# Optimization experiments

Hardware: AMD Instinct MI355X
Metric: run time of the kernel (lower is better)

The kernel has to match this reference:

```python
import jax, jax.numpy as jnp
import numpy as np
from jax import lax

EPS = 1e-5
NBIT = 127.0  # 8-bit symmetric: 2^(8-1)-1

def ste_round(x):
    return x + lax.stop_gradient(jnp.round(x) - x)

def quant_act(x, rng_max):
    # symmetric fake-quant of activations with learned per-cluster range
    s = rng_max / NBIT
    xq = jnp.clip(ste_round(x / s), -NBIT, NBIT) * s
    return xq, s

def fold_bn(w, gamma, beta, mean, var):
    std = jnp.sqrt(var + EPS)
    scale = gamma / std
    w_f = w * scale[:, None, None, None]
    b_f = beta - mean * scale
    return w_f, b_f

def quant_weight(w):
    # per-output-channel symmetric quant
    s = jnp.max(jnp.abs(w), axis=(1, 2, 3), keepdims=True) / NBIT
    wq = jnp.clip(ste_round(w / s), -NBIT, NBIT) * s
    return wq, s.reshape(-1)

def conv(x, w, stride=1, groups=1, pad=0):
    return lax.conv_general_dilated(
        x, w, window_strides=(stride, stride),
        padding=((pad, pad), (pad, pad)),
        dimension_numbers=('NCHW', 'OIHW', 'NCHW'),
        feature_group_count=groups)

def setup_inputs() -> dict:
    key = jax.random.key(0)
    ks = jax.random.split(key, 24)
    B, Cin, H, W = 64, 96, 28, 28
    Cmid, Cout, NC = 576, 96, 4
    d = {}
    d['x'] = jax.random.normal(ks[0], (B, Cin, H, W), dtype=jnp.float32)
    # conv1: 1x1 expansion
    d['w1'] = jax.random.normal(ks[1], (Cmid, Cin, 1, 1), jnp.float32) * 0.1
    d['g1'] = jax.random.uniform(ks[2], (Cmid,), minval=0.5, maxval=1.5)
    d['b1'] = jax.random.normal(ks[3], (Cmid,)) * 0.1
    d['m1'] = jax.random.normal(ks[4], (Cmid,)) * 0.1
    d['v1'] = jax.random.uniform(ks[5], (Cmid,), minval=0.5, maxval=1.5)
    # conv2: 3x3 depthwise
    d['w2'] = jax.random.normal(ks[6], (Cmid, 1, 3, 3), jnp.float32) * 0.1
    d['g2'] = jax.random.uniform(ks[7], (Cmid,), minval=0.5, maxval=1.5)
    d['b2'] = jax.random.normal(ks[8], (Cmid,)) * 0.1
    d['m2'] = jax.random.normal(ks[9], (Cmid,)) * 0.1
    d['v2'] = jax.random.uniform(ks[10], (Cmid,), minval=0.5, maxval=1.5)
    # conv3: 1x1 projection
    d['w3'] = jax.random.normal(ks[11], (Cout, Cmid, 1, 1), jnp.float32) * 0.1
    d['g3'] = jax.random.uniform(ks[12], (Cout,), minval=0.5, maxval=1.5)
    d['b3'] = jax.random.normal(ks[13], (Cout,)) * 0.1
    d['m3'] = jax.random.normal(ks[14], (Cout,)) * 0.1
    d['v3'] = jax.random.uniform(ks[15], (Cout,), minval=0.5, maxval=1.5)
    # per-cluster learned activation ranges for the 4 QuantAct modules
    d['r0'] = jax.random.uniform(ks[16], (NC,), minval=2.0, maxval=8.0)
    d['r1'] = jax.random.uniform(ks[17], (NC,), minval=2.0, maxval=8.0)
    d['r2'] = jax.random.uniform(ks[18], (NC,), minval=2.0, maxval=8.0)
    d['r3'] = jax.random.uniform(ks[19], (NC,), minval=2.0, maxval=8.0)
    d['cluster'] = 2
    return d

def reference(x, w1, g1, b1, m1, v1, w2, g2, b2, m2, v2,
              w3, g3, b3, m3, v3, r0, r1, r2, r3, cluster):
    identity = x  # residual path (in==out, stride==1)
    # QuantAct -> conv1 (BN-folded, per-channel quant) -> ReLU6
    xq, s0 = quant_act(x, r0[cluster])
    w1f, bf1 = fold_bn(w1, g1, b1, m1, v1)
    w1q, ws1 = quant_weight(w1f)
    y = conv(xq, w1q) + bf1[None, :, None, None]
    y = jnp.clip(y, 0.0, 6.0)
    # QuantAct1 -> depthwise conv2 -> ReLU6
    yq, s1 = quant_act(y, r1[cluster])
    w2f, bf2 = fold_bn(w2, g2, b2, m2, v2)
    w2q, ws2 = quant_weight(w2f)
    y = conv(yq, w2q, stride=1, groups=w2.shape[0], pad=1) + bf2[None, :, None, None]
    y = jnp.clip(y, 0.0, 6.0)
    # QuantAct2 -> conv3 projection
    yq, s2 = quant_act(y, r2[cluster])
    w3f, bf3 = fold_bn(w3, g3, b3, m3, v3)
    w3q, ws3 = quant_weight(w3f)
    y = conv(yq, w3q) + bf3[None, :, None, None]
    # residual add, then int32 requant
    y = y + identity
    out, s3 = quant_act(y, r3[cluster])
    return out, s3
```

## Files before the change

kernel.cpp:

```cpp
#include <hip/hip_runtime.h>
#include <cstdint>
#include <cstddef>

typedef int   v4i __attribute__((ext_vector_type(4)));
typedef float v4f __attribute__((ext_vector_type(4)));
typedef unsigned int u32;

constexpr int B_   = 64;
constexpr int CIN  = 96;
constexpr int P_   = 784;
constexpr int CMID = 576;
constexpr int COUT = 96;
constexpr int NOUT = B_ * COUT * P_;
constexpr float NBITF = 127.0f;
constexpr float EPSF  = 1e-5f;
constexpr float MAGICF = 12582912.0f;
constexpr int   BIASI  = 0x4B400000;

constexpr int XKD = 36;
constexpr int XBD = 13 * XKD * 64;

__device__ __forceinline__ int dot3(u32 a, u32 w, int acc) {
#if __has_builtin(__builtin_amdgcn_sdot4)
    return __builtin_amdgcn_sdot4((int)a, (int)w, acc, false);
#else
    return acc + (int)(signed char)(a)        * (int)(signed char)(w)
               + (int)(signed char)(a >> 8)   * (int)(signed char)(w >> 8)
               + (int)(signed char)(a >> 16)  * (int)(signed char)(w >> 16);
#endif
}

__device__ __forceinline__ void tr4(u32 S0, u32 S1, u32 S2, u32 S3, u32 O[4]) {
    u32 u01 = __builtin_amdgcn_perm(S1, S0, 0x05010400u);
    u32 u23 = __builtin_amdgcn_perm(S3, S2, 0x05010400u);
    u32 v01 = __builtin_amdgcn_perm(S1, S0, 0x07030602u);
    u32 v23 = __builtin_amdgcn_perm(S3, S2, 0x07030602u);
    O[0] = __builtin_amdgcn_perm(u23, u01, 0x05040100u);
    O[1] = __builtin_amdgcn_perm(u23, u01, 0x07060302u);
    O[2] = __builtin_amdgcn_perm(v23, v01, 0x05040100u);
    O[3] = __builtin_amdgcn_perm(v23, v01, 0x07060302u);
}

__device__ __forceinline__ u32 pack4(u32 t0, u32 t1, u32 t2, u32 t3) {
    u32 p01 = __builtin_amdgcn_perm(t1, t0, 0x05010400u);
    u32 p23 = __builtin_amdgcn_perm(t3, t2, 0x05010400u);
    return __builtin_amdgcn_perm(p23, p01, 0x05040100u);
}

__global__ __launch_bounds__(256)
void prep_all(const float* __restrict__ x,
              const float* __restrict__ w1, const float* __restrict__ g1,
              const float* __restrict__ b1, const float* __restrict__ m1,
              const float* __restrict__ v1,
              const float* __restrict__ w2, const float* __restrict__ g2,
              const float* __restrict__ b2, const float* __restrict__ m2,
              const float* __restrict__ v2,
              const float* __restrict__ w3, const float* __restrict__ g3,
              const float* __restrict__ b3, const float* __restrict__ m3,
              const float* __restrict__ v3,
              const float* __restrict__ r0, const int* __restrict__ cluster,
              u32* __restrict__ x8t,
              int8_t* __restrict__ w1qp, float* __restrict__ ws1, float* __restrict__ bf1,
              v4i* __restrict__ w2pk, float* __restrict__ ws2, float* __restrict__ bf2,
              int8_t* __restrict__ w3qp, float* __restrict__ ws3, float* __restrict__ bf3)
{
    __shared__ u32 T[112 * 37];
    int tid = threadIdx.x;

    if (blockIdx.x < 448) {
        int pt0 = blockIdx.x % 7, b = blockIdx.x / 7;
        float inv_s0 = NBITF / r0[cluster[0]];

        for (int i = tid; i < 112 * 12; i += 256) {
            int row = i / 12, cpad = i - row * 12;
            T[row * 37 + 24 + cpad] = 0u;
        }
        for (int u = tid; u < 24 * 28; u += 256) {
            int pq = u % 28, icq = u / 28;
            int pxb = pt0 * 112 + pq * 4;
            int q[4][4];
            #pragma unroll
            for (int j = 0; j < 4; j++) {
                v4f xv = *(const v4f*)(x + ((size_t)b * CIN + icq * 4 + j) * P_ + pxb);
                #pragma unroll
                for (int i = 0; i < 4; i++)
                    q[j][i] = (int)fminf(fmaxf(rintf(xv[i] * inv_s0), -127.f), 127.f);
            }
            #pragma unroll
            for (int i = 0; i < 4; i++) {
                u32 t0 = __builtin_amdgcn_perm((u32)q[1][i], (u32)q[0][i], 0x00000400u);
                u32 t1 = __builtin_amdgcn_perm((u32)q[3][i], (u32)q[2][i], 0x00000400u);
                T[(pq * 4 + i) * 37 + icq] = __builtin_amdgcn_perm(t1, t0, 0x05040100u);
            }
        }
        __syncthreads();
        u32* gb = x8t + (size_t)b * XBD;
        for (int i = tid; i < XKD * 112; i += 256) {
            int icq = i / 112, pxo = i - icq * 112;
            int px = pt0 * 112 + pxo;
            gb[(((px >> 6) * XKD) + icq) * 64 + (px & 63)] = T[pxo * 37 + icq];
        }
        return;
    }

    int lane = tid & 63, wv = tid >> 6;
    int blk = (blockIdx.x - 448) * 4 + wv;

    const float *w, *g, *bb, *mm, *vv;
    int oc, K, which;
    if (blk < CMID)            { which = 0; w = w1; g = g1; bb = b1; mm = m1; vv = v1; oc = blk;            K = CIN;  }
    else if (blk < 2 * CMID)   { which = 1; w = w2; g = g2; bb = b2; mm = m2; vv = v2; oc = blk - CMID;     K = 9;    }
    else                       { which = 2; w = w3; g = g3; bb = b3; mm = m3; vv = v3; oc = blk - 2 * CMID; K = CMID; }

    float scale = g[oc] / sqrtf(vv[oc] + EPSF);

    float mx = 0.f;
    for (int k = lane; k < K; k += 64)
        mx = fmaxf(mx, fabsf(w[oc * K + k] * scale));
    #pragma unroll
    for (int off = 1; off < 64; off <<= 1)
        mx = fmaxf(mx, __shfl_xor(mx, off));

    float s = mx / NBITF;

    int myq = 0;
    for (int k = lane; k < K; k += 64) {
        float wf = w[oc * K + k] * scale;
        float q  = fminf(fmaxf(rintf(wf / s), -127.f), 127.f);
        if (which == 0)      w1qp[oc * 144 + k] = (int8_t)q;
        else if (which == 1) myq = (int)q;
        else                 w3qp[oc * 592 + k] = (int8_t)q;
    }
    if (which == 0 && lane < 12)
        ((u32*)(w1qp + oc * 144))[24 + lane] = 0u;
    if (which == 1) {
        u32 qq[9];
        #pragma unroll
        for (int t = 0; t < 9; t++) qq[t] = (u32)__shfl(myq, t, 64) & 0xffu;
        if (lane == 0) {
            v4i pk;
            pk[0] = (int)(qq[0] | (qq[1] << 8) | (qq[2] << 16));
            pk[1] = (int)(qq[3] | (qq[4] << 8) | (qq[5] << 16));
            pk[2] = (int)(qq[6] | (qq[7] << 8) | (qq[8] << 16));
            pk[3] = 0;
            w2pk[oc] = pk;
        }
    }
    if (lane == 0) {
        float bf = bb[oc] - mm[oc] * scale;
        if (which == 0)      { ws1[oc] = s; bf1[oc] = bf; }
        else if (which == 1) { ws2[oc] = s; bf2[oc] = bf; }
        else                 { ws3[oc] = s; bf3[oc] = bf; }
    }
}

__global__ __launch_bounds__(256)
void conv12v2(const u32* __restrict__ x8t, const int8_t* __restrict__ w1qp,
              const float* __restrict__ ws1, const float* __restrict__ bf1,
              const v4i* __restrict__ w2pk, const float* __restrict__ ws2,
              const float* __restrict__ bf2,
              const float* __restrict__ r0, const float* __restrict__ r1,
              const float* __restrict__ r2, const int* __restrict__ cluster,
              u32* __restrict__ y2px)
{
    __shared__ u32 y1w[192 * 34];

    int tid = threadIdx.x, b = blockIdx.y;
    int mt = blockIdx.x % 3, pt = blockIdx.x / 3;
    int p0 = pt * 64;
    int lane = tid & 63, wv = tid >> 6;
    int n = lane & 15, q4 = lane >> 4;
    int ocw = mt * 192 + wv * 48;

    int   c      = cluster[0];
    float s0     = r0[c] / NBITF;
    float s1     = r1[c] / NBITF;
    float inv_s1 = NBITF / r1[c];
    float inv_s2 = NBITF / r2[c];
    int   u1i    = (int)fminf(rintf(6.f * inv_s1), 127.f);
    int   u2i    = (int)fminf(rintf(6.f * inv_s2), 127.f);

    const u32* xb = x8t + (size_t)b * XBD;
    int abase[8];
    #pragma unroll
    for (int jm = 0; jm < 8; jm++) {
        int px = p0 - 32 + 16 * jm + n;
        px = min(max(px, 0), P_ - 1);
        abase[jm] = ((px >> 6) * XKD) * 64 + (px & 63);
    }

    v4i acc[3][8];
    #pragma unroll
    for (int jn = 0; jn < 3; jn++)
        #pragma unroll
        for (int jm = 0; jm < 8; jm++) acc[jn][jm] = (v4i){0, 0, 0, 0};

    const v4i* w4 = (const v4i*)w1qp;
    #pragma unroll
    for (int ks = 0; ks < 2; ks++) {
        v4i bfr[3];
        #pragma unroll
        for (int jn = 0; jn < 3; jn++) {
            int oc = ocw + 16 * jn + n;
            bfr[jn] = w4[oc * 9 + ks * 4 + q4];
        }
        int kb = (16 * ks + 4 * q4) * 64;
        #pragma unroll
        for (int jm = 0; jm < 8; jm++) {
            u32 d0 = xb[abase[jm] + kb];
            u32 d1 = xb[abase[jm] + kb + 64];
            u32 d2 = xb[abase[jm] + kb + 128];
            u32 d3 = xb[abase[jm] + kb + 192];
            v4i afr = (v4i){(int)d0, (int)d1, (int)d2, (int)d3};
            #pragma unroll
            for (int jn = 0; jn < 3; jn++)
                acc[jn][jm] = __builtin_amdgcn_mfma_i32_16x16x64_i8(afr, bfr[jn], acc[jn][jm], 0, 0, 0);
        }
    }

    #pragma unroll
    for (int jn = 0; jn < 3; jn++) {
        int   oc  = ocw + 16 * jn + n;
        int   chl = wv * 48 + 16 * jn + n;
        float scv = s0 * ws1[oc] * inv_s1;
        float bbv = bf1[oc] * inv_s1;
        #pragma unroll
        for (int jm = 0; jm < 8; jm++) {
            u32 t[4];
            #pragma unroll
            for (int r = 0; r < 4; r++) {
                int wpx = p0 - 32 + 16 * jm + 4 * q4 + r;
                float f = fmaf((float)acc[jn][jm][r], scv, bbv) + MAGICF;
                int v = min(max(__float_as_int(f), BIASI), BIASI + u1i);
                t[r] = ((unsigned)wpx < (unsigned)P_) ? (u32)v : (u32)BIASI;
            }
            y1w[chl * 34 + 4 * jm + q4] = pack4(t[0], t[1], t[2], t[3]);
        }
    }
    __syncthreads();

    int d0g = p0 >> 2;
    #pragma unroll
    for (int it = 0; it < 12; it++) {
        int u   = tid + 256 * it;
        int chl = u >> 4, dq = u & 15;
        int d   = d0g + dq;
        int gcol = d % 7;
        int base = chl * 34 + 8 + dq;

        u32 M[3][3];
        #pragma unroll
        for (int rr = 0; rr < 3; rr++) {
            int o = (rr - 1) * 7;
            M[rr][0] = (gcol == 0) ? 0u : y1w[base + o - 1];
            M[rr][1] = y1w[base + o];
            M[rr][2] = (gcol == 6) ? 0u : y1w[base + o + 1];
        }
        int ch = mt * 192 + chl;
        v4i wpk = w2pk[ch];
        int a0 = 0, a1 = 0, a2 = 0, a3 = 0;
        #pragma unroll
        for (int rr = 0; rr < 3; rr++) {
            u32 Dm1 = M[rr][0], D = M[rr][1], Dp1 = M[rr][2];
            u32 pk = (u32)((rr == 0) ? wpk[0] : (rr == 1) ? wpk[1] : wpk[2]);
            a0 = dot3(__builtin_amdgcn_alignbyte(D, Dm1, 3), pk, a0);
            a1 = dot3(D, pk, a1);
            a2 = dot3(__builtin_amdgcn_alignbyte(Dp1, D, 1), pk, a2);
            a3 = dot3(__builtin_amdgcn_alignbyte(Dp1, D, 2), pk, a3);
        }
        float scv = s1 * ws2[ch] * inv_s2;
        float bbv = bf2[ch] * inv_s2;
        int aa[4] = {a0, a1, a2, a3};
        u32 tq[4];
        #pragma unroll
        for (int i = 0; i < 4; i++) {
            float f = fmaf((float)aa[i], scv, bbv) + MAGICF;
            tq[i] = (u32)min(max(__float_as_int(f), BIASI), BIASI + u2i);
        }
        if (d < 196)
            y2px[(size_t)(b * CMID + ch) * 196 + d] = pack4(tq[0], tq[1], tq[2], tq[3]);
    }
}

__global__ __launch_bounds__(256)
void conv3s(const u32* __restrict__ y2px, const int8_t* __restrict__ w3qp,
            const float* __restrict__ ws3, const float* __restrict__ bf3,
            const float* __restrict__ x, const float* __restrict__ r2,
            const float* __restrict__ r3, const int* __restrict__ cluster,
            float* __restrict__ out)
{
    __shared__ u32 Bsh[144 * 67];

    int tid = threadIdx.x, b = blockIdx.y, pt = blockIdx.x;
    int p0d = pt * 16;

    int   c      = cluster[0];
    float s2     = r2[c] / NBITF;
    float s3     = r3[c] / NBITF;
    float inv_s3 = NBITF / r3[c];

    for (int u = tid; u < 2304; u += 256) {
        int pxq = u & 15, chq = u >> 4;
        u32 S[4];
        #pragma unroll
        for (int r = 0; r < 4; r++) {
            int col = min(p0d + pxq, 195);
            S[r] = y2px[(size_t)(b * CMID + 4 * chq + r) * 196 + col];
        }
        u32 O[4];
        tr4(S[0], S[1], S[2], S[3], O);
        #pragma unroll
        for (int k = 0; k < 4; k++)
            Bsh[chq * 67 + 4 * pxq + k] = O[k];
    }
    __syncthreads();

    int lane = tid & 63, wv = tid >> 6;
    int n = lane & 15, q4 = lane >> 4;
    int pxl = wv * 16 + n;

    v4i acc[6];
    #pragma unroll
    for (int i = 0; i < 6; i++) acc[i] = (v4i){0, 0, 0, 0};

    #pragma unroll
    for (int ks = 0; ks < 9; ks++) {
        int kr = 16 * ks + 4 * q4;
        u32 b0 = Bsh[(kr + 0) * 67 + pxl];
        u32 b1 = Bsh[(kr + 1) * 67 + pxl];
        u32 b2 = Bsh[(kr + 2) * 67 + pxl];
        u32 b3 = Bsh[(kr + 3) * 67 + pxl];
        v4i bfr = (v4i){(int)b0, (int)b1, (int)b2, (int)b3};
        #pragma unroll
        for (int i = 0; i < 6; i++) {
            v4i afr = *(const v4i*)(w3qp + (size_t)(i * 16 + n) * 592 + ks * 64 + q4 * 16);
            acc[i] = __builtin_amdgcn_mfma_i32_16x16x64_i8(afr, bfr, acc[i], 0, 0, 0);
        }
    }

    int px = pt * 64 + pxl;
    if (px < P_) {
        #pragma unroll
        for (int i = 0; i < 6; i++) {
            #pragma unroll
            for (int r = 0; r < 4; r++) {
                int oc = i * 16 + q4 * 4 + r;
                size_t gi = (size_t)(b * COUT + oc) * P_ + px;
                float v  = (float)acc[i][r] * (s2 * ws3[oc]) + bf3[oc] + x[gi];
                float f  = fmaf(v, inv_s3, MAGICF);
                int lvl  = min(max(__float_as_int(f) - BIASI, -127), 127);
                out[gi]  = (float)lvl * s3;
            }
        }
    }
    if (pt == 0 && b == 0 && tid == 0)
        out[NOUT] = s3;
}

extern "C" void kernel_launch(void* const* d_in, const int* in_sizes, int n_in,
                              void* d_out, int out_size, void* d_ws, size_t ws_size,
                              hipStream_t stream)
{
    const float* x  = (const float*)d_in[0];
    const float* w1 = (const float*)d_in[1];
    const float* g1 = (const float*)d_in[2];
    const float* b1 = (const float*)d_in[3];
    const float* m1 = (const float*)d_in[4];
    const float* v1 = (const float*)d_in[5];
    const float* w2 = (const float*)d_in[6];
    const float* g2 = (const float*)d_in[7];
    const float* b2 = (const float*)d_in[8];
    const float* m2 = (const float*)d_in[9];
    const float* v2 = (const float*)d_in[10];
    const float* w3 = (const float*)d_in[11];
    const float* g3 = (const float*)d_in[12];
    const float* b3 = (const float*)d_in[13];
    const float* m3 = (const float*)d_in[14];
    const float* v3 = (const float*)d_in[15];
    const float* r0 = (const float*)d_in[16];
    const float* r1 = (const float*)d_in[17];
    const float* r2 = (const float*)d_in[18];
    const float* r3 = (const float*)d_in[19];
    const int*   cl = (const int*)d_in[20];

    float* out = (float*)d_out;

    char*  ws  = (char*)d_ws;
    size_t off = 0;
    auto carve = [&](size_t bytes) {
        size_t cur = off;
        off = (off + bytes + 255) & ~(size_t)255;
        return (void*)(ws + cur);
    };
    int8_t* w1qp = (int8_t*)carve((size_t)CMID * 144);
    float*  ws1  = (float*)carve(CMID * 4);
    float*  bf1  = (float*)carve(CMID * 4);
    v4i*    w2pk = (v4i*)carve((size_t)CMID * 16);
    float*  ws2  = (float*)carve(CMID * 4);
    float*  bf2  = (float*)carve(CMID * 4);
    int8_t* w3qp = (int8_t*)carve((size_t)COUT * 592);
    float*  ws3  = (float*)carve(COUT * 4);
    float*  bf3  = (float*)carve(COUT * 4);
    u32*    x8t  = (u32*)carve((size_t)B_ * XBD * 4);
    u32*    y2px = (u32*)carve((size_t)B_ * CMID * 196 * 4);
    (void)ws_size; (void)in_sizes; (void)n_in; (void)out_size;

    prep_all<<<dim3(760), dim3(256), 0, stream>>>(
        x, w1, g1, b1, m1, v1, w2, g2, b2, m2, v2, w3, g3, b3, m3, v3,
        r0, cl, x8t,
        w1qp, ws1, bf1, w2pk, ws2, bf2, w3qp, ws3, bf3);

    conv12v2<<<dim3(39, B_), dim3(256), 0, stream>>>(
        x8t, w1qp, ws1, bf1, w2pk, ws2, bf2, r0, r1, r2, cl, y2px);

    conv3s<<<dim3(13, B_), dim3(256), 0, stream>>>(
        y2px, w3qp, ws3, bf3, x, r2, r3, cl, out);
}
```

Measured before the change: 188.8 us.

## Retile fused conv1/depthwise by image row pairs and store MFMA-ready packed layouts

The int8 activation buffers are rewritten in an interleaved layout where each lane fetches a full 16-byte MFMA fragment with one load instead of four strided dword loads. The fused conv1+depthwise kernel now tiles by two image rows (with halo rows) rather than 64-pixel chunks. The depthwise pass slides a register window along each row and emits output already transposed into the conv3 B-fragment layout. That removes the shared-memory transpose stage and its barrier from the projection kernel. The cost is a slightly larger grid, a halo of two extra rows per pair, and a more complex store pattern.

```diff
diff --git a/kernel.cpp b/kernel.cpp
--- a/kernel.cpp
+++ b/kernel.cpp
@@ -17,8 +17,8 @@
 constexpr float MAGICF = 12582912.0f;
 constexpr int   BIASI  = 0x4B400000;
 
-constexpr int XKD = 36;
-constexpr int XBD = 13 * XKD * 64;
+constexpr int XB4 = 13 * 8 * 64;
+constexpr int YB4 = 13 * 36 * 64;
 
 __device__ __forceinline__ int dot3(u32 a, u32 w, int acc) {
 #if __has_builtin(__builtin_amdgcn_sdot4)
@@ -59,7 +59,7 @@
               const float* __restrict__ b3, const float* __restrict__ m3,
               const float* __restrict__ v3,
               const float* __restrict__ r0, const int* __restrict__ cluster,
-              u32* __restrict__ x8t,
+              u32* __restrict__ x8t2,
               int8_t* __restrict__ w1qp, float* __restrict__ ws1, float* __restrict__ bf1,
               v4i* __restrict__ w2pk, float* __restrict__ ws2, float* __restrict__ bf2,
               int8_t* __restrict__ w3qp, float* __restrict__ ws3, float* __restrict__ bf3)
@@ -71,9 +71,9 @@
         int pt0 = blockIdx.x % 7, b = blockIdx.x / 7;
         float inv_s0 = NBITF / r0[cluster[0]];
 
-        for (int i = tid; i < 112 * 12; i += 256) {
-            int row = i / 12, cpad = i - row * 12;
-            T[row * 37 + 24 + cpad] = 0u;
+        for (int i = tid; i < 112 * 8; i += 256) {
+            int row = i >> 3, c = 24 + (i & 7);
+            T[row * 37 + c] = 0u;
         }
         for (int u = tid; u < 24 * 28; u += 256) {
             int pq = u % 28, icq = u / 28;
@@ -94,11 +94,12 @@
             }
         }
         __syncthreads();
-        u32* gb = x8t + (size_t)b * XBD;
-        for (int i = tid; i < XKD * 112; i += 256) {
+        u32* gb = x8t2 + (size_t)b * XB4 * 4;
+        for (int i = tid; i < 32 * 112; i += 256) {
             int icq = i / 112, pxo = i - icq * 112;
             int px = pt0 * 112 + pxo;
-            gb[(((px >> 6) * XKD) + icq) * 64 + (px & 63)] = T[pxo * 37 + icq];
+            gb[(((px >> 6) * 8 + (icq >> 2)) * 64 + (px & 63)) * 4 + (icq & 3)] =
+                T[pxo * 37 + icq];
         }
         return;
     }
@@ -155,19 +156,21 @@
 }
 
 __global__ __launch_bounds__(256)
-void conv12v2(const u32* __restrict__ x8t, const int8_t* __restrict__ w1qp,
-              const float* __restrict__ ws1, const float* __restrict__ bf1,
-              const v4i* __restrict__ w2pk, const float* __restrict__ ws2,
-              const float* __restrict__ bf2,
-              const float* __restrict__ r0, const float* __restrict__ r1,
-              const float* __restrict__ r2, const int* __restrict__ cluster,
-              u32* __restrict__ y2px)
+void conv12r(const u32* __restrict__ x8t2, const int8_t* __restrict__ w1qp,
+             const float* __restrict__ ws1, const float* __restrict__ bf1,
+             const v4i* __restrict__ w2pk, const float* __restrict__ ws2,
+             const float* __restrict__ bf2,
+             const float* __restrict__ r0, const float* __restrict__ r1,
+             const float* __restrict__ r2, const int* __restrict__ cluster,
+             v4i* __restrict__ y2t)
 {
-    __shared__ u32 y1w[192 * 34];
+    __shared__ u32 y1w[192 * 29];
+    __shared__ u32 y2s[192 * 15];
 
     int tid = threadIdx.x, b = blockIdx.y;
-    int mt = blockIdx.x % 3, pt = blockIdx.x / 3;
-    int p0 = pt * 64;
+    int mt = blockIdx.x / 14, rt = blockIdx.x - mt * 14;
+    int R0 = 2 * rt;
+    int W0 = (R0 - 1) * 28;
     int lane = tid & 63, wv = tid >> 6;
     int n = lane & 15, q4 = lane >> 4;
     int ocw = mt * 192 + wv * 48;
@@ -180,41 +183,35 @@
     int   u1i    = (int)fminf(rintf(6.f * inv_s1), 127.f);
     int   u2i    = (int)fminf(rintf(6.f * inv_s2), 127.f);
 
-    const u32* xb = x8t + (size_t)b * XBD;
-    int abase[8];
-    #pragma unroll
-    for (int jm = 0; jm < 8; jm++) {
-        int px = p0 - 32 + 16 * jm + n;
+    const v4i* xb = (const v4i*)x8t2 + (size_t)b * XB4;
+    int pb[7];
+    #pragma unroll
+    for (int jm = 0; jm < 7; jm++) {
+        int px = W0 + 16 * jm + n;
         px = min(max(px, 0), P_ - 1);
-        abase[jm] = ((px >> 6) * XKD) * 64 + (px & 63);
-    }
-
-    v4i acc[3][8];
+        pb[jm] = (px >> 6) * 512 + (px & 63);
+    }
+
+    v4i acc[3][7];
     #pragma unroll
     for (int jn = 0; jn < 3; jn++)
         #pragma unroll
-        for (int jm = 0; jm < 8; jm++) acc[jn][jm] = (v4i){0, 0, 0, 0};
+        for (int jm = 0; jm < 7; jm++) acc[jn][jm] = (v4i){0, 0, 0, 0};
 
     const v4i* w4 = (const v4i*)w1qp;
     #pragma unroll
     for (int ks = 0; ks < 2; ks++) {
-        v4i bfr[3];
-        #pragma unroll
-        for (int jn = 0; jn < 3; jn++) {
-            int oc = ocw + 16 * jn + n;
-            bfr[jn] = w4[oc * 9 + ks * 4 + q4];
-        }
-        int kb = (16 * ks + 4 * q4) * 64;
-        #pragma unroll
-        for (int jm = 0; jm < 8; jm++) {
-            u32 d0 = xb[abase[jm] + kb];
-            u32 d1 = xb[abase[jm] + kb + 64];
-            u32 d2 = xb[abase[jm] + kb + 128];
-            u32 d3 = xb[abase[jm] + kb + 192];
-            v4i afr = (v4i){(int)d0, (int)d1, (int)d2, (int)d3};
+        v4i bw[3];
+        #pragma unroll
+        for (int jn = 0; jn < 3; jn++)
+            bw[jn] = w4[(ocw + 16 * jn + n) * 9 + 4 * ks + q4];
+        int go = (4 * ks + q4) * 64;
+        #pragma unroll
+        for (int jm = 0; jm < 7; jm++) {
+            v4i af = xb[pb[jm] + go];
             #pragma unroll
             for (int jn = 0; jn < 3; jn++)
-                acc[jn][jm] = __builtin_amdgcn_mfma_i32_16x16x64_i8(afr, bfr[jn], acc[jn][jm], 0, 0, 0);
+                acc[jn][jm] = __builtin_amdgcn_mfma_i32_16x16x64_i8(af, bw[jn], acc[jn][jm], 0, 0, 0);
         }
     }
 
@@ -225,99 +222,112 @@
         float scv = s0 * ws1[oc] * inv_s1;
         float bbv = bf1[oc] * inv_s1;
         #pragma unroll
-        for (int jm = 0; jm < 8; jm++) {
+        for (int jm = 0; jm < 7; jm++) {
             u32 t[4];
             #pragma unroll
             for (int r = 0; r < 4; r++) {
-                int wpx = p0 - 32 + 16 * jm + 4 * q4 + r;
                 float f = fmaf((float)acc[jn][jm][r], scv, bbv) + MAGICF;
-                int v = min(max(__float_as_int(f), BIASI), BIASI + u1i);
-                t[r] = ((unsigned)wpx < (unsigned)P_) ? (u32)v : (u32)BIASI;
+                t[r] = (u32)min(max(__float_as_int(f), BIASI), BIASI + u1i);
             }
-            y1w[chl * 34 + 4 * jm + q4] = pack4(t[0], t[1], t[2], t[3]);
+            int dw = 4 * jm + q4;
+            u32 pk = pack4(t[0], t[1], t[2], t[3]);
+            pk = ((unsigned)(W0 + 4 * dw) < (unsigned)P_) ? pk : 0u;
+            y1w[chl * 29 + dw] = pk;
         }
     }
     __syncthreads();
 
-    int d0g = p0 >> 2;
-    #pragma unroll
-    for (int it = 0; it < 12; it++) {
-        int u   = tid + 256 * it;
-        int chl = u >> 4, dq = u & 15;
-        int d   = d0g + dq;
-        int gcol = d % 7;
-        int base = chl * 34 + 8 + dq;
-
-        u32 M[3][3];
-        #pragma unroll
-        for (int rr = 0; rr < 3; rr++) {
-            int o = (rr - 1) * 7;
-            M[rr][0] = (gcol == 0) ? 0u : y1w[base + o - 1];
-            M[rr][1] = y1w[base + o];
-            M[rr][2] = (gcol == 6) ? 0u : y1w[base + o + 1];
-        }
-        int ch = mt * 192 + chl;
+    for (int u = tid; u < 384; u += 256) {
+        int chl = u >> 1, orow = u & 1;
+        int ch  = mt * 192 + chl;
+        int rb  = chl * 29 + orow * 7;
+
         v4i wpk = w2pk[ch];
-        int a0 = 0, a1 = 0, a2 = 0, a3 = 0;
-        #pragma unroll
-        for (int rr = 0; rr < 3; rr++) {
-            u32 Dm1 = M[rr][0], D = M[rr][1], Dp1 = M[rr][2];
-            u32 pk = (u32)((rr == 0) ? wpk[0] : (rr == 1) ? wpk[1] : wpk[2]);
-            a0 = dot3(__builtin_amdgcn_alignbyte(D, Dm1, 3), pk, a0);
-            a1 = dot3(D, pk, a1);
-            a2 = dot3(__builtin_amdgcn_alignbyte(Dp1, D, 1), pk, a2);
-            a3 = dot3(__builtin_amdgcn_alignbyte(Dp1, D, 2), pk, a3);
-        }
+        u32 pk0 = (u32)wpk[0], pk1 = (u32)wpk[1], pk2 = (u32)wpk[2];
         float scv = s1 * ws2[ch] * inv_s2;
         float bbv = bf2[ch] * inv_s2;
-        int aa[4] = {a0, a1, a2, a3};
-        u32 tq[4];
+
+        u32 M0 = 0, M1 = 0, M2 = 0;
+        u32 D0 = y1w[rb], D1 = y1w[rb + 7], D2 = y1w[rb + 14];
+        #pragma unroll
+        for (int xq = 0; xq < 7; xq++) {
+            u32 N0, N1, N2;
+            if (xq < 6) {
+                N0 = y1w[rb + xq + 1];
+                N1 = y1w[rb + 7 + xq + 1];
+                N2 = y1w[rb + 14 + xq + 1];
+            } else { N0 = N1 = N2 = 0u; }
+
+            int a0, a1, a2, a3;
+            a0 = dot3(__builtin_amdgcn_alignbyte(D0, M0, 3), pk0, 0);
+            a0 = dot3(__builtin_amdgcn_alignbyte(D1, M1, 3), pk1, a0);
+            a0 = dot3(__builtin_amdgcn_alignbyte(D2, M2, 3), pk2, a0);
+            a1 = dot3(D0, pk0, 0);
+            a1 = dot3(D1, pk1, a1);
+            a1 = dot3(D2, pk2, a1);
+            a2 = dot3(__builtin_amdgcn_alignbyte(N0, D0, 1), pk0, 0);
+            a2 = dot3(__builtin_amdgcn_alignbyte(N1, D1, 1), pk1, a2);
+            a2 = dot3(__builtin_amdgcn_alignbyte(N2, D2, 1), pk2, a2);
+            a3 = dot3(__builtin_amdgcn_alignbyte(N0, D0, 2), pk0, 0);
+            a3 = dot3(__builtin_amdgcn_alignbyte(N1, D1, 2), pk1, a3);
+            a3 = dot3(__builtin_amdgcn_alignbyte(N2, D2, 2), pk2, a3);
+
+            int aa[4] = {a0, a1, a2, a3};
+            u32 tq[4];
+            #pragma unroll
+            for (int i = 0; i < 4; i++) {
+                float f = fmaf((float)aa[i], scv, bbv) + MAGICF;
+                tq[i] = (u32)min(max(__float_as_int(f), BIASI), BIASI + u2i);
+            }
+            y2s[chl * 15 + orow * 7 + xq] = pack4(tq[0], tq[1], tq[2], tq[3]);
+
+            M0 = D0; M1 = D1; M2 = D2;
+            D0 = N0; D1 = N1; D2 = N2;
+        }
+    }
+    __syncthreads();
+
+    v4i* yb = y2t + (size_t)b * YB4;
+    for (int u = tid; u < 168; u += 256) {
+        int kgl = u / 14, d = u - kgl * 14;
+        u32 O[4][4];
+        #pragma unroll
+        for (int j = 0; j < 4; j++) {
+            int cb = (16 * kgl + 4 * j) * 15 + d;
+            tr4(y2s[cb], y2s[cb + 15], y2s[cb + 30], y2s[cb + 45], O[j]);
+        }
+        int gpx0 = R0 * 28 + 4 * d;
         #pragma unroll
         for (int i = 0; i < 4; i++) {
-            float f = fmaf((float)aa[i], scv, bbv) + MAGICF;
-            tq[i] = (u32)min(max(__float_as_int(f), BIASI), BIASI + u2i);
-        }
-        if (d < 196)
-            y2px[(size_t)(b * CMID + ch) * 196 + d] = pack4(tq[0], tq[1], tq[2], tq[3]);
+            int gp = gpx0 + i;
+            v4i val = (v4i){(int)O[0][i], (int)O[1][i], (int)O[2][i], (int)O[3][i]};
+            yb[((gp >> 6) * 36 + mt * 12 + kgl) * 64 + (gp & 63)] = val;
+        }
     }
 }
 
 __global__ __launch_bounds__(256)
-void conv3s(const u32* __restrict__ y2px, const int8_t* __restrict__ w3qp,
+void conv3d(const v4i* __restrict__ y2t, const int8_t* __restrict__ w3qp,
             const float* __restrict__ ws3, const float* __restrict__ bf3,
             const float* __restrict__ x, const float* __restrict__ r2,
             const float* __restrict__ r3, const int* __restrict__ cluster,
             float* __restrict__ out)
 {
-    __shared__ u32 Bsh[144 * 67];
-
     int tid = threadIdx.x, b = blockIdx.y, pt = blockIdx.x;
-    int p0d = pt * 16;
+    int lane = tid & 63, wv = tid >> 6;
+    int n = lane & 15, q4 = lane >> 4;
+    int pxl = wv * 16 + n;
+    int px  = pt * 64 + pxl;
+    int pxc = min(px, P_ - 1);
 
     int   c      = cluster[0];
     float s2     = r2[c] / NBITF;
     float s3     = r3[c] / NBITF;
     float inv_s3 = NBITF / r3[c];
 
-    for (int u = tid; u < 2304; u += 256) {
-        int pxq = u & 15, chq = u >> 4;
-        u32 S[4];
-        #pragma unroll
-        for (int r = 0; r < 4; r++) {
-            int col = min(p0d + pxq, 195);
-            S[r] = y2px[(size_t)(b * CMID + 4 * chq + r) * 196 + col];
-        }
-        u32 O[4];
-        tr4(S[0], S[1], S[2], S[3], O);
-        #pragma unroll
-        for (int k = 0; k < 4; k++)
-            Bsh[chq * 67 + 4 * pxq + k] = O[k];
-    }
-    __syncthreads();
-
-    int lane = tid & 63, wv = tid >> 6;
-    int n = lane & 15, q4 = lane >> 4;
-    int pxl = wv * 16 + n;
+    const v4i* yb  = y2t + (size_t)b * YB4;
+    int pb3 = (pxc >> 6) * (36 * 64) + (pxc & 63);
+    const v4i* w34 = (const v4i*)w3qp;
 
     v4i acc[6];
     #pragma unroll
@@ -325,20 +335,14 @@
 
     #pragma unroll
     for (int ks = 0; ks < 9; ks++) {
-        int kr = 16 * ks + 4 * q4;
-        u32 b0 = Bsh[(kr + 0) * 67 + pxl];
-        u32 b1 = Bsh[(kr + 1) * 67 + pxl];
-        u32 b2 = Bsh[(kr + 2) * 67 + pxl];
-        u32 b3 = Bsh[(kr + 3) * 67 + pxl];
-        v4i bfr = (v4i){(int)b0, (int)b1, (int)b2, (int)b3};
+        v4i bfr = yb[pb3 + (4 * ks + q4) * 64];
         #pragma unroll
         for (int i = 0; i < 6; i++) {
-            v4i afr = *(const v4i*)(w3qp + (size_t)(i * 16 + n) * 592 + ks * 64 + q4 * 16);
+            v4i afr = w34[(i * 16 + n) * 37 + 4 * ks + q4];
             acc[i] = __builtin_amdgcn_mfma_i32_16x16x64_i8(afr, bfr, acc[i], 0, 0, 0);
         }
     }
 
-    int px = pt * 64 + pxl;
     if (px < P_) {
         #pragma unroll
         for (int i = 0; i < 6; i++) {
@@ -401,18 +405,18 @@
     int8_t* w3qp = (int8_t*)carve((size_t)COUT * 592);
     float*  ws3  = (float*)carve(COUT * 4);
     float*  bf3  = (float*)carve(COUT * 4);
-    u32*    x8t  = (u32*)carve((size_t)B_ * XBD * 4);
-    u32*    y2px = (u32*)carve((size_t)B_ * CMID * 196 * 4);
+    u32*    x8t2 = (u32*)carve((size_t)B_ * XB4 * 16);
+    v4i*    y2t  = (v4i*)carve((size_t)B_ * YB4 * 16);
     (void)ws_size; (void)in_sizes; (void)n_in; (void)out_size;
 
     prep_all<<<dim3(760), dim3(256), 0, stream>>>(
         x, w1, g1, b1, m1, v1, w2, g2, b2, m2, v2, w3, g3, b3, m3, v3,
-        r0, cl, x8t,
+        r0, cl, x8t2,
         w1qp, ws1, bf1, w2pk, ws2, bf2, w3qp, ws3, bf3);
 
-    conv12v2<<<dim3(39, B_), dim3(256), 0, stream>>>(
-        x8t, w1qp, ws1, bf1, w2pk, ws2, bf2, r0, r1, r2, cl, y2px);
-
-    conv3s<<<dim3(13, B_), dim3(256), 0, stream>>>(
-        y2px, w3qp, ws3, bf3, x, r2, r3, cl, out);
-}
+    conv12r<<<dim3(42, B_), dim3(256), 0, stream>>>(
+        x8t2, w1qp, ws1, bf1, w2pk, ws2, bf2, r0, r1, r2, cl, y2t);
+
+    conv3d<<<dim3(13, B_), dim3(256), 0, stream>>>(
+        y2t, w3qp, ws3, bf3, x, r2, r3, cl, out);
+}
```

Result: faster. 177.6 us (-5.9%).
